# Optimization experiments

Measured on AMD Instinct MI355X. Metric: run time of the kernel, lower is better.

Reference implementation:

```python
import jax, jax.numpy as jnp
import numpy as np

B, S, D, HID, H, VOCAB, DFF = 4, 2048, 512, 512, 8, 32000, 2048
DK = HID // H   # per-head Q/K dim
DV = D // H     # per-head V dim


def sinusoidal_pe(L, d):
    pos = jnp.arange(L, dtype=jnp.float32)[:, None]
    i = jnp.arange(d, dtype=jnp.float32)[None, :]
    ang = pos / jnp.power(jnp.float32(10000.0), i / d)
    return jnp.where(jnp.arange(d)[None, :] % 2 == 0, jnp.sin(ang), jnp.cos(ang))  # [L, d]


def layer_norm(x, gamma, beta, eps=1e-5):
    mu = jnp.mean(x, axis=-1, keepdims=True)
    var = jnp.mean((x - mu) ** 2, axis=-1, keepdims=True)
    return (x - mu) * jax.lax.rsqrt(var + eps) * gamma + beta


def setup_inputs() -> dict:
    key = jax.random.key(0)
    ks = jax.random.split(key, 24)
    n = lambda k, shape, fan: jax.random.normal(k, shape, dtype=jnp.float32) / np.sqrt(fan)
    inp = {
        'x': jax.random.randint(ks[0], (B, S), 0, VOCAB),
        'emb': n(ks[1], (VOCAB, D), D),
        'WfQ': n(ks[2], (D, HID), D), 'bfQ': jnp.zeros((HID,), jnp.float32),
        'WfK': n(ks[3], (D, HID), D), 'bfK': jnp.zeros((HID,), jnp.float32),
        'WfV': n(ks[4], (D, D), D),   'bfV': jnp.zeros((D,), jnp.float32),
        'WQ': n(ks[5], (H, HID, DK), HID), 'bQ': jnp.zeros((H, DK), jnp.float32),
        'WK': n(ks[6], (H, HID, DK), HID), 'bK': jnp.zeros((H, DK), jnp.float32),
        'WV': n(ks[7], (H, D, DV), D),     'bV': jnp.zeros((H, DV), jnp.float32),
        'Wo': n(ks[8], (D, D), D),   'bo': jnp.zeros((D,), jnp.float32),
        'W1': n(ks[9], (D, DFF), D), 'b1': jnp.zeros((DFF,), jnp.float32),
        'W2': n(ks[10], (DFF, D), DFF), 'b2': jnp.zeros((D,), jnp.float32),
        'gamma': jnp.ones((D,), jnp.float32), 'beta': jnp.zeros((D,), jnp.float32),
    }
    return inp


def reference(x, emb, WfQ, bfQ, WfK, bfK, WfV, bfV, WQ, bQ, WK, bK, WV, bV,
              Wo, bo, W1, b1, W2, b2, gamma, beta):
    z = emb[x] + sinusoidal_pe(x.shape[1], D)[None]            # [B,S,D]
    Q = z @ WfQ + bfQ                                           # [B,S,HID]
    K = z @ WfK + bfK
    V = z @ WfV + bfV                                           # [B,S,D]
    # per-head projections (batched equivalent of the per-head Linear loop)
    Qh = jnp.einsum('bsd,hdk->bhsk', Q, WQ) + bQ[None, :, None, :]  # [B,H,S,DK]
    Kh = jnp.einsum('bsd,hdk->bhsk', K, WK) + bK[None, :, None, :]
    Vh = jnp.einsum('bsd,hdv->bhsv', V, WV) + bV[None, :, None, :]  # [B,H,S,DV]
    scores = jnp.einsum('bhqk,bhsk->bhqs', Qh, Kh) / np.sqrt(DK)    # [B,H,S,S]
    attn = jax.nn.softmax(scores, axis=-1)
    heads = jnp.einsum('bhqs,bhsv->bhqv', attn, Vh)                 # [B,H,S,DV]
    concat = heads.transpose(0, 2, 1, 3).reshape(x.shape[0], x.shape[1], D)
    attn_out = concat @ Wo + bo
    a = layer_norm(attn_out + z, gamma, beta)
    ffn = jax.nn.relu(a @ W1 + b1) @ W2 + b2
    out = layer_norm(ffn + a, gamma, beta)   # same (shared) LayerNorm params, as in source
    return jax.nn.relu(out)
```

## Files before the change

kernel.cpp:

```cpp
#include <hip/hip_runtime.h>
#include <math.h>

typedef __bf16 bf16;
typedef __bf16 bf16x8 __attribute__((ext_vector_type(8)));
typedef __bf16 bf16x4 __attribute__((ext_vector_type(4)));
typedef _Float16 f16;
typedef _Float16 f16x8 __attribute__((ext_vector_type(8)));
typedef _Float16 f16x4 __attribute__((ext_vector_type(4)));
typedef _Float16 f16x2 __attribute__((ext_vector_type(2)));
typedef __fp16 h16x2 __attribute__((ext_vector_type(2)));
typedef float f32x4 __attribute__((ext_vector_type(4)));
typedef unsigned int u32;

#define S_LEN 2048
#define QSCALE 0.18033688011112042f
#define FIXEDMAX 8.0f

__device__ __forceinline__ void gload_lds16(const void* g, void* l) {
  __builtin_amdgcn_global_load_lds((const __attribute__((address_space(1))) u32*)g,
                                   (__attribute__((address_space(3))) u32*)l, 16, 0, 0);
}

__global__ __launch_bounds__(256) void embed_pe(const int* __restrict__ x,
    const float* __restrict__ emb, float* __restrict__ zf, bf16* __restrict__ zb)
{
  const int row = blockIdx.x;
  const int s = row & (S_LEN - 1);
  const int tok = x[row];
  const float* e = emb + (size_t)tok * 512;
  float* zr = zf + (size_t)row * 512;
  bf16* zbr = zb + (size_t)row * 512;
  for (int i = threadIdx.x; i < 512; i += 256) {
    float invf = __expf((float)i * (-9.210340371976184f / 512.0f));
    float ang = (float)s * invf;
    float pe = (i & 1) ? __cosf(ang) : __sinf(ang);
    float v = e[i] + pe;
    zr[i] = v;
    zbr[i] = (bf16)v;
  }
}

__global__ __launch_bounds__(256) void conv_all(
    const float* __restrict__ WfQ, const float* __restrict__ WfK, const float* __restrict__ WfV,
    const float* __restrict__ WQ, const float* __restrict__ WK, const float* __restrict__ WV,
    const float* __restrict__ Wo, const float* __restrict__ W1, const float* __restrict__ W2,
    bf16* __restrict__ wfqp, bf16* __restrict__ wfkp, bf16* __restrict__ wfvp,
    bf16* __restrict__ wqt, bf16* __restrict__ wkt, bf16* __restrict__ wvt,
    bf16* __restrict__ wot, bf16* __restrict__ w1t, bf16* __restrict__ w2t)
{
  int gid = blockIdx.x * 256 + threadIdx.x;
  int y = blockIdx.y;
  if (y < 3) {
    if (gid >= 262144) return;
    const float* in = y == 0 ? WfQ : (y == 1 ? WfK : WfV);
    bf16* out = y == 0 ? wfqp : (y == 1 ? wfkp : wfvp);
    out[gid] = (bf16)in[gid];
  } else if (y < 6) {
    if (gid >= 262144) return;
    const float* in = y == 3 ? WQ : (y == 4 ? WK : WV);
    bf16* out = y == 3 ? wqt : (y == 4 ? wkt : wvt);
    float scale = y == 3 ? QSCALE : 1.0f;
    int r = gid & 511, t = gid >> 9, c = t & 63, h = t >> 6;
    out[gid] = (bf16)(in[((size_t)(h * 512 + r)) * 64 + c] * scale);
  } else if (y == 6) {
    if (gid >= 262144) return;
    int r = gid & 511, c = gid >> 9;
    wot[gid] = (bf16)Wo[r * 512 + c];
  } else if (y == 7) {
    int r = gid & 511, c = gid >> 9;
    w1t[gid] = (bf16)W1[r * 2048 + c];
  } else {
    int r = gid & 2047, c = gid >> 11;
    w2t[gid] = (bf16)W2[r * 512 + c];
  }
}

__global__ __launch_bounds__(256) void bias_comb(
    const float* __restrict__ bfQ, const float* __restrict__ bfK, const float* __restrict__ bfV,
    const float* __restrict__ WQ, const float* __restrict__ WK, const float* __restrict__ WV,
    const float* __restrict__ bQ, const float* __restrict__ bK, const float* __restrict__ bV,
    float* __restrict__ bc)
{
  int n = blockIdx.x * 4 + (threadIdx.x >> 6);
  int lane = threadIdx.x & 63;
  int z = n >> 9, hk = n & 511, h = hk >> 6, k = hk & 63;
  const float* bf = z == 0 ? bfQ : (z == 1 ? bfK : bfV);
  const float* W  = z == 0 ? WQ  : (z == 1 ? WK  : WV);
  const float* bH = z == 0 ? bQ  : (z == 1 ? bK  : bV);
  float s = 0.f;
  for (int e = lane; e < 512; e += 64)
    s += bf[e] * W[((size_t)h * 512 + e) * 64 + k];
  #pragma unroll
  for (int m = 1; m < 64; m <<= 1) s += __shfl_xor(s, m, 64);
  if (lane == 0) {
    float v = s + bH[h * 64 + k];
    if (z == 0) v *= QSCALE;
    bc[n] = v;
  }
}

__global__ __launch_bounds__(256) void gemm_comb(
    const bf16* __restrict__ wqt, const bf16* __restrict__ wkt, const bf16* __restrict__ wvt,
    const bf16* __restrict__ wfqp, const bf16* __restrict__ wfkp, const bf16* __restrict__ wfvp,
    bf16* __restrict__ wc)
{
  __shared__ bf16 As[128 * 32];
  __shared__ bf16 Bs[64 * 32];
  const int z = blockIdx.z;
  const bf16* A  = z == 0 ? wqt : (z == 1 ? wkt : wvt);
  const bf16* Bt = z == 0 ? wfqp : (z == 1 ? wfkp : wfvp);
  bf16* outb = wc + (size_t)z * 262144;
  const int tid = threadIdx.x;
  const int wave = tid >> 6, lane = tid & 63, quad = lane >> 4, l16 = lane & 15;
  const int row0 = blockIdx.x * 128, col0 = blockIdx.y * 64;
  const int wm = wave >> 1, wn = wave & 1;
  f32x4 acc[4][2] = {};

  for (int kk = 0; kk < 512; kk += 32) {
    __syncthreads();
    #pragma unroll
    for (int r = 0; r < 2; r++) {
      int c = r * 256 + tid;
      gload_lds16(A + (size_t)(row0 + (c >> 2)) * 512 + kk + (c & 3) * 8, As + c * 8);
    }
    gload_lds16(Bt + (size_t)(col0 + (tid >> 2)) * 512 + kk + (tid & 3) * 8, Bs + tid * 8);
    __syncthreads();
    bf16x8 af[4], bfr[2];
    #pragma unroll
    for (int i = 0; i < 4; i++)
      af[i] = *(const bf16x8*)(As + (wm * 64 + i * 16 + l16) * 32 + quad * 8);
    #pragma unroll
    for (int i = 0; i < 2; i++)
      bfr[i] = *(const bf16x8*)(Bs + (wn * 32 + i * 16 + l16) * 32 + quad * 8);
    #pragma unroll
    for (int mt = 0; mt < 4; mt++)
      #pragma unroll
      for (int nt = 0; nt < 2; nt++)
        acc[mt][nt] = __builtin_amdgcn_mfma_f32_16x16x32_bf16(af[mt], bfr[nt], acc[mt][nt], 0, 0, 0);
  }
  #pragma unroll
  for (int nt = 0; nt < 2; nt++) {
    int col = col0 + wn * 32 + nt * 16 + l16;
    #pragma unroll
    for (int mt = 0; mt < 4; mt++) {
      int rowb = row0 + wm * 64 + mt * 16 + quad * 4;
      #pragma unroll
      for (int i = 0; i < 4; i++)
        outb[(size_t)(rowb + i) * 512 + col] = (bf16)acc[mt][nt][i];
    }
  }
}

__global__ __launch_bounds__(256) void gemm_bt(
    const bf16* __restrict__ A, const bf16* __restrict__ Bt,
    const float* __restrict__ bias, bf16* __restrict__ outb,
    int M, int N, int K, int relu)
{
  __shared__ bf16 As[128 * 32];
  __shared__ bf16 Bs[128 * 32];
  const int tid = threadIdx.x;
  const int wave = tid >> 6, lane = tid & 63, quad = lane >> 4, l16 = lane & 15;
  const int row0 = blockIdx.x * 128, col0 = blockIdx.y * 128;
  const int wm = wave >> 1, wn = wave & 1;
  f32x4 acc[4][4] = {};

  for (int kk = 0; kk < K; kk += 32) {
    __syncthreads();
    #pragma unroll
    for (int r = 0; r < 2; r++) {
      int c = r * 256 + tid;
      gload_lds16(A + (size_t)(row0 + (c >> 2)) * K + kk + (c & 3) * 8, As + c * 8);
    }
    #pragma unroll
    for (int r = 0; r < 2; r++) {
      int c = r * 256 + tid;
      gload_lds16(Bt + (size_t)(col0 + (c >> 2)) * K + kk + (c & 3) * 8, Bs + c * 8);
    }
    __syncthreads();
    bf16x8 af[4], bfr[4];
    #pragma unroll
    for (int i = 0; i < 4; i++)
      af[i] = *(const bf16x8*)(As + (wm * 64 + i * 16 + l16) * 32 + quad * 8);
    #pragma unroll
    for (int i = 0; i < 4; i++)
      bfr[i] = *(const bf16x8*)(Bs + (wn * 64 + i * 16 + l16) * 32 + quad * 8);
    #pragma unroll
    for (int mt = 0; mt < 4; mt++)
      #pragma unroll
      for (int nt = 0; nt < 4; nt++)
        acc[mt][nt] = __builtin_amdgcn_mfma_f32_16x16x32_bf16(af[mt], bfr[nt], acc[mt][nt], 0, 0, 0);
  }

  #pragma unroll
  for (int nt = 0; nt < 4; nt++) {
    int col = col0 + wn * 64 + nt * 16 + l16;
    float bv = bias[col];
    #pragma unroll
    for (int mt = 0; mt < 4; mt++) {
      int rowb = row0 + wm * 64 + mt * 16 + quad * 4;
      #pragma unroll
      for (int i = 0; i < 4; i++) {
        float v = acc[mt][nt][i] + bv;
        if (relu) v = fmaxf(v, 0.f);
        outb[(size_t)(rowb + i) * N + col] = (bf16)v;
      }
    }
  }
}

__global__ __launch_bounds__(256) void gemm_qkv(
    const bf16* __restrict__ A, const bf16* __restrict__ Bt,
    const float* __restrict__ bias, f16* __restrict__ qk, f16* __restrict__ Vt)
{
  __shared__ bf16 As[128 * 32];
  __shared__ bf16 Bs[128 * 32];
  const int tid = threadIdx.x;
  const int wave = tid >> 6, lane = tid & 63, quad = lane >> 4, l16 = lane & 15;
  const int row0 = blockIdx.x * 128, col0 = blockIdx.y * 128;
  const int wm = wave >> 1, wn = wave & 1;
  f32x4 acc[4][4] = {};

  for (int kk = 0; kk < 512; kk += 32) {
    __syncthreads();
    #pragma unroll
    for (int r = 0; r < 2; r++) {
      int c = r * 256 + tid;
      gload_lds16(A + (size_t)(row0 + (c >> 2)) * 512 + kk + (c & 3) * 8, As + c * 8);
    }
    #pragma unroll
    for (int r = 0; r < 2; r++) {
      int c = r * 256 + tid;
      gload_lds16(Bt + (size_t)(col0 + (c >> 2)) * 512 + kk + (c & 3) * 8, Bs + c * 8);
    }
    __syncthreads();
    bf16x8 af[4], bfr[4];
    #pragma unroll
    for (int i = 0; i < 4; i++)
      af[i] = *(const bf16x8*)(As + (wm * 64 + i * 16 + l16) * 32 + quad * 8);
    #pragma unroll
    for (int i = 0; i < 4; i++)
      bfr[i] = *(const bf16x8*)(Bs + (wn * 64 + i * 16 + l16) * 32 + quad * 8);
    #pragma unroll
    for (int mt = 0; mt < 4; mt++)
      #pragma unroll
      for (int nt = 0; nt < 4; nt++)
        acc[mt][nt] = __builtin_amdgcn_mfma_f32_16x16x32_bf16(af[mt], bfr[nt], acc[mt][nt], 0, 0, 0);
  }

  #pragma unroll
  for (int nt = 0; nt < 4; nt++) {
    int col = col0 + wn * 64 + nt * 16 + l16;
    float bv = bias[col];
    if (col < 1024) {
      #pragma unroll
      for (int mt = 0; mt < 4; mt++) {
        int rowb = row0 + wm * 64 + mt * 16 + quad * 4;
        #pragma unroll
        for (int i = 0; i < 4; i++)
          qk[(size_t)(rowb + i) * 1024 + col] = (f16)(acc[mt][nt][i] + bv);
      }
    } else {
      int h = (col - 1024) >> 6, dv = col & 63;
      #pragma unroll
      for (int mt = 0; mt < 4; mt++) {
        int rowb = row0 + wm * 64 + mt * 16 + quad * 4;
        int b = rowb >> 11, s = rowb & 2047;
        f16x4 vv;
        #pragma unroll
        for (int i = 0; i < 4; i++) vv[i] = (f16)(acc[mt][nt][i] + bv);
        *(f16x4*)(Vt + ((size_t)((b * 8 + h) * 64 + dv)) * 2048 + s) = vv;
      }
    }
  }
}

__global__ __launch_bounds__(256) void gemm_part(
    const bf16* __restrict__ A, const bf16* __restrict__ Bt,
    float* __restrict__ Pa, float* __restrict__ Pb, int N, int K, int Kh)
{
  __shared__ bf16 As[128 * 32];
  __shared__ bf16 Bs[128 * 32];
  const int tid = threadIdx.x;
  const int wave = tid >> 6, lane = tid & 63, quad = lane >> 4, l16 = lane & 15;
  const int row0 = blockIdx.x * 128, col0 = blockIdx.y * 128;
  const int wm = wave >> 1, wn = wave & 1;
  const int kk0 = blockIdx.z * Kh;
  float* P = blockIdx.z ? Pb : Pa;
  f32x4 acc[4][4] = {};

  for (int kk = kk0; kk < kk0 + Kh; kk += 32) {
    __syncthreads();
    #pragma unroll
    for (int r = 0; r < 2; r++) {
      int c = r * 256 + tid;
      gload_lds16(A + (size_t)(row0 + (c >> 2)) * K + kk + (c & 3) * 8, As + c * 8);
    }
    #pragma unroll
    for (int r = 0; r < 2; r++) {
      int c = r * 256 + tid;
      gload_lds16(Bt + (size_t)(col0 + (c >> 2)) * K + kk + (c & 3) * 8, Bs + c * 8);
    }
    __syncthreads();
    bf16x8 af[4], bfr[4];
    #pragma unroll
    for (int i = 0; i < 4; i++)
      af[i] = *(const bf16x8*)(As + (wm * 64 + i * 16 + l16) * 32 + quad * 8);
    #pragma unroll
    for (int i = 0; i < 4; i++)
      bfr[i] = *(const bf16x8*)(Bs + (wn * 64 + i * 16 + l16) * 32 + quad * 8);
    #pragma unroll
    for (int mt = 0; mt < 4; mt++)
      #pragma unroll
      for (int nt = 0; nt < 4; nt++)
        acc[mt][nt] = __builtin_amdgcn_mfma_f32_16x16x32_bf16(af[mt], bfr[nt], acc[mt][nt], 0, 0, 0);
  }

  #pragma unroll
  for (int nt = 0; nt < 4; nt++) {
    int col = col0 + wn * 64 + nt * 16 + l16;
    #pragma unroll
    for (int mt = 0; mt < 4; mt++) {
      int rowb = row0 + wm * 64 + mt * 16 + quad * 4;
      #pragma unroll
      for (int i = 0; i < 4; i++)
        P[(size_t)(rowb + i) * N + col] = acc[mt][nt][i];
    }
  }
}

__global__ __launch_bounds__(256) void flash_attn(
    const f16* __restrict__ qk, const f16* __restrict__ Vt,
    bf16* __restrict__ Op, float* __restrict__ Rp)
{
  __shared__ f16 Ks[2][4096];
  __shared__ f16 Vs[2][4096];
  const int bh = blockIdx.y, b = bh >> 3, h = bh & 7;
  const int q0 = blockIdx.x * 128;
  const int half = blockIdx.z;
  const int tid = threadIdx.x;
  const int wave = tid >> 6, lane = tid & 63, quad = lane >> 4, l16 = lane & 15;

  const f16* Qb = qk + ((size_t)b * S_LEN) * 1024 + h * 64;
  const f16* Kb = Qb + 512;
  const f16* Vtb = Vt + ((size_t)bh * 64) * 2048;
  const int key0 = half * 1024;

  f16x8 qf[2][2];
  #pragma unroll
  for (int f = 0; f < 2; f++) {
    int qrow = q0 + wave * 32 + f * 16 + l16;
    #pragma unroll
    for (int kh = 0; kh < 2; kh++)
      qf[f][kh] = *(const f16x8*)(Qb + (size_t)qrow * 1024 + kh * 32 + quad * 8);
  }

  f32x4 O[2][4] = {};
  f32x4 Osum[2] = {};
  const f16x4 onesA = {(f16)1.f, (f16)1.f, (f16)1.f, (f16)1.f};
  const int swz = l16 & 7;

  f16x8 kreg[2], vreg[2];
  const int srow = tid >> 3, soff = tid & 7;
  const int srow1 = srow + 32;

  {
    int kb = key0;
    kreg[0] = *(const f16x8*)(Kb + (size_t)(kb + srow) * 1024 + soff * 8);
    vreg[0] = *(const f16x8*)(Vtb + (size_t)srow * 2048 + kb + soff * 8);
    kreg[1] = *(const f16x8*)(Kb + (size_t)(kb + srow1) * 1024 + soff * 8);
    vreg[1] = *(const f16x8*)(Vtb + (size_t)srow1 * 2048 + kb + soff * 8);
  }

  for (int c = 0; c < 16; c++) {
    f16* KsB = Ks[c & 1];
    f16* VsB = Vs[c & 1];
    *(f16x8*)(KsB + srow * 64 + ((soff ^ (srow & 7)) * 8)) = kreg[0];
    *(f16x8*)(VsB + srow * 64 + ((soff ^ (srow & 7)) * 8)) = vreg[0];
    *(f16x8*)(KsB + srow1 * 64 + ((soff ^ (srow1 & 7)) * 8)) = kreg[1];
    *(f16x8*)(VsB + srow1 * 64 + ((soff ^ (srow1 & 7)) * 8)) = vreg[1];
    __syncthreads();
    if (c < 15) {
      int kb = key0 + (c + 1) * 64;
      kreg[0] = *(const f16x8*)(Kb + (size_t)(kb + srow) * 1024 + soff * 8);
      vreg[0] = *(const f16x8*)(Vtb + (size_t)srow * 2048 + kb + soff * 8);
      kreg[1] = *(const f16x8*)(Kb + (size_t)(kb + srow1) * 1024 + soff * 8);
      vreg[1] = *(const f16x8*)(Vtb + (size_t)srow1 * 2048 + kb + soff * 8);
    }

    #pragma unroll
    for (int nt = 0; nt < 4; nt++) {
      const f16* kp = KsB + (nt * 16 + l16) * 64;
      f16x8 kf0 = *(const f16x8*)(kp + ((quad ^ swz) * 8));
      f16x8 kf1 = *(const f16x8*)(kp + (((4 + quad) ^ swz) * 8));
      f16x4 pf[2];
      #pragma unroll
      for (int f = 0; f < 2; f++) {
        f32x4 a = {};
        a = __builtin_amdgcn_mfma_f32_16x16x32_f16(kf0, qf[f][0], a, 0, 0, 0);
        a = __builtin_amdgcn_mfma_f32_16x16x32_f16(kf1, qf[f][1], a, 0, 0, 0);
        float e0 = exp2f(a[0] - FIXEDMAX);
        float e1 = exp2f(a[1] - FIXEDMAX);
        float e2 = exp2f(a[2] - FIXEDMAX);
        float e3 = exp2f(a[3] - FIXEDMAX);
        h16x2 lo = __builtin_amdgcn_cvt_pkrtz(e0, e1);
        h16x2 hi = __builtin_amdgcn_cvt_pkrtz(e2, e3);
        f16x2 lo2 = __builtin_bit_cast(f16x2, lo);
        f16x2 hi2 = __builtin_bit_cast(f16x2, hi);
        pf[f] = __builtin_shufflevector(lo2, hi2, 0, 1, 2, 3);
        Osum[f] = __builtin_amdgcn_mfma_f32_16x16x16f16(onesA, pf[f], Osum[f], 0, 0, 0);
      }
      int vchunk = nt * 2 + (quad >> 1);
      #pragma unroll
      for (int mt = 0; mt < 4; mt++) {
        const f16* vp = VsB + (mt * 16 + l16) * 64 + ((vchunk ^ swz) * 8) + (quad & 1) * 4;
        f16x4 vf = *(const f16x4*)vp;
        #pragma unroll
        for (int f = 0; f < 2; f++)
          O[f][mt] = __builtin_amdgcn_mfma_f32_16x16x16f16(vf, pf[f], O[f][mt], 0, 0, 0);
      }
    }
    __syncthreads();
  }

  #pragma unroll
  for (int f = 0; f < 2; f++) {
    bf16* ob = (f == 0 ? (bf16*)&Ks[0][0] : (bf16*)&Vs[0][0]) + wave * 1152;
    #pragma unroll
    for (int mt = 0; mt < 4; mt++)
      #pragma unroll
      for (int i = 0; i < 4; i++)
        ob[l16 * 72 + mt * 16 + quad * 4 + i] = (bf16)O[f][mt][i];
  }
  asm volatile("s_waitcnt lgkmcnt(0)" ::: "memory");
  const size_t obase = (size_t)(half * 32 + bh) * 2048;
  #pragma unroll
  for (int f = 0; f < 2; f++) {
    bf16* ob = (f == 0 ? (bf16*)&Ks[0][0] : (bf16*)&Vs[0][0]) + wave * 1152;
    int row = lane >> 2, dvb = (lane & 3) * 16;
    bf16x8 o0 = *(const bf16x8*)(ob + row * 72 + dvb);
    bf16x8 o1 = *(const bf16x8*)(ob + row * 72 + dvb + 8);
    size_t g = (obase + q0 + wave * 32 + f * 16 + row) * 64 + dvb;
    *(bf16x8*)(Op + g) = o0;
    *(bf16x8*)(Op + g + 8) = o1;
    if (quad == f)
      Rp[obase + q0 + wave * 32 + f * 16 + l16] = Osum[f][0];
  }
}

__global__ __launch_bounds__(256) void attn_merge(const bf16* __restrict__ Op,
    const float* __restrict__ Rp, bf16* __restrict__ concat)
{
  int t = blockIdx.x * 256 + threadIdx.x;
  int dv4 = t & 15, s = (t >> 4) & 2047, bh = t >> 15;
  int rb = bh * 2048 + s;
  float r = Rp[rb] + Rp[65536 + rb];
  float inv = 1.f / r;
  size_t ia = ((size_t)bh * 2048 + s) * 64 + dv4 * 4;
  bf16x4 a = *(const bf16x4*)(Op + ia);
  bf16x4 c = *(const bf16x4*)(Op + 4194304ull + ia);
  bf16x4 o;
  #pragma unroll
  for (int i = 0; i < 4; i++) o[i] = (bf16)(((float)a[i] + (float)c[i]) * inv);
  int b = bh >> 3, h = bh & 7;
  *(bf16x4*)(concat + ((size_t)(b * 2048 + s)) * 512 + h * 64 + dv4 * 4) = o;
}

__global__ __launch_bounds__(256) void ln_merge(const float* __restrict__ Pa,
    const float* __restrict__ Pb, const float* __restrict__ badd,
    const float* __restrict__ resid, const float* __restrict__ gamma,
    const float* __restrict__ beta, float* __restrict__ outf,
    bf16* __restrict__ outb, int relu)
{
  const int row = blockIdx.x * 4 + (threadIdx.x >> 6);
  const int lane = threadIdx.x & 63;
  const size_t base = (size_t)row * 512;
  const float4* pa = (const float4*)(Pa + base);
  const float4* pb = (const float4*)(Pb + base);
  const float4* rr = (const float4*)(resid + base);
  const float4* bb = (const float4*)badd;
  float4 A0 = pa[lane], A1 = pa[lane + 64];
  float4 B0 = pb[lane], B1 = pb[lane + 64];
  float4 R0 = rr[lane], R1 = rr[lane + 64];
  float4 C0 = bb[lane], C1 = bb[lane + 64];
  float4 v0 = {A0.x+B0.x+R0.x+C0.x, A0.y+B0.y+R0.y+C0.y, A0.z+B0.z+R0.z+C0.z, A0.w+B0.w+R0.w+C0.w};
  float4 v1 = {A1.x+B1.x+R1.x+C1.x, A1.y+B1.y+R1.y+C1.y, A1.z+B1.z+R1.z+C1.z, A1.w+B1.w+R1.w+C1.w};
  float s = v0.x + v0.y + v0.z + v0.w + v1.x + v1.y + v1.z + v1.w;
  #pragma unroll
  for (int m = 1; m < 64; m <<= 1) s += __shfl_xor(s, m, 64);
  float mu = s * (1.f / 512.f);
  float d0 = v0.x - mu, d1 = v0.y - mu, d2 = v0.z - mu, d3 = v0.w - mu;
  float d4 = v1.x - mu, d5 = v1.y - mu, d6 = v1.z - mu, d7 = v1.w - mu;
  float q = d0*d0 + d1*d1 + d2*d2 + d3*d3 + d4*d4 + d5*d5 + d6*d6 + d7*d7;
  #pragma unroll
  for (int m = 1; m < 64; m <<= 1) q += __shfl_xor(q, m, 64);
  float rs = rsqrtf(q * (1.f / 512.f) + 1e-5f);
  const float4* gp = (const float4*)gamma;
  const float4* bp = (const float4*)beta;
  float4 g0 = gp[lane], g1 = gp[lane + 64];
  float4 b0 = bp[lane], b1 = bp[lane + 64];
  float y0 = d0 * rs * g0.x + b0.x, y1 = d1 * rs * g0.y + b0.y;
  float y2 = d2 * rs * g0.z + b0.z, y3 = d3 * rs * g0.w + b0.w;
  float y4 = d4 * rs * g1.x + b1.x, y5 = d5 * rs * g1.y + b1.y;
  float y6 = d6 * rs * g1.z + b1.z, y7 = d7 * rs * g1.w + b1.w;
  if (relu) {
    y0 = fmaxf(y0, 0.f); y1 = fmaxf(y1, 0.f); y2 = fmaxf(y2, 0.f); y3 = fmaxf(y3, 0.f);
    y4 = fmaxf(y4, 0.f); y5 = fmaxf(y5, 0.f); y6 = fmaxf(y6, 0.f); y7 = fmaxf(y7, 0.f);
  }
  float4* op = (float4*)(outf + base);
  float4 o0 = {y0, y1, y2, y3}, o1 = {y4, y5, y6, y7};
  op[lane] = o0;
  op[lane + 64] = o1;
  if (outb) {
    bf16x4 c0 = {(bf16)y0, (bf16)y1, (bf16)y2, (bf16)y3};
    bf16x4 c1 = {(bf16)y4, (bf16)y5, (bf16)y6, (bf16)y7};
    *(bf16x4*)(outb + base + lane * 4) = c0;
    *(bf16x4*)(outb + base + 256 + lane * 4) = c1;
  }
}

extern "C" void kernel_launch(void* const* d_in, const int* in_sizes, int n_in,
                              void* d_out, int out_size, void* d_ws, size_t ws_size,
                              hipStream_t stream)
{
  const int*   x    = (const int*)  d_in[0];
  const float* emb  = (const float*)d_in[1];
  const float* WfQ  = (const float*)d_in[2];
  const float* bfQv = (const float*)d_in[3];
  const float* WfK  = (const float*)d_in[4];
  const float* bfKv = (const float*)d_in[5];
  const float* WfV  = (const float*)d_in[6];
  const float* bfVv = (const float*)d_in[7];
  const float* WQ   = (const float*)d_in[8];
  const float* bQ   = (const float*)d_in[9];
  const float* WK   = (const float*)d_in[10];
  const float* bK   = (const float*)d_in[11];
  const float* WV   = (const float*)d_in[12];
  const float* bV   = (const float*)d_in[13];
  const float* Wo   = (const float*)d_in[14];
  const float* bo   = (const float*)d_in[15];
  const float* W1   = (const float*)d_in[16];
  const float* b1   = (const float*)d_in[17];
  const float* W2   = (const float*)d_in[18];
  const float* b2   = (const float*)d_in[19];
  const float* gamma= (const float*)d_in[20];
  const float* beta = (const float*)d_in[21];
  float* out = (float*)d_out;

  char* ws = (char*)d_ws;
  const size_t MB = 1024ull * 1024;
  float* zf   = (float*)(ws);
  bf16*  bz   = (bf16*) (ws + 16 * MB);
  f16*   qkh  = (f16*)  (ws + 24 * MB);
  f16*   Vt   = (f16*)  (ws + 40 * MB);
  bf16*  Op   = (bf16*) (ws + 48 * MB);
  float* Rp   = (float*)(ws + 80 * MB);
  bf16*  concat = (bf16*)(ws + 82 * MB);
  float* PaW  = (float*)(ws + 48 * MB);
  float* PbW  = (float*)(ws + 64 * MB);
  bf16*  ffn1 = (bf16*) (ws + 24 * MB);
  float* Pa2  = (float*)(ws + 56 * MB);
  float* Pb2  = (float*)(ws + 72 * MB);
  char* wp = ws + 90 * MB;
  bf16* wfqp = (bf16*)(wp);
  bf16* wfkp = (bf16*)(wp + 512 * 1024);
  bf16* wfvp = (bf16*)(wp + 1024 * 1024);
  bf16* wqt  = (bf16*)(wp + 1536 * 1024);
  bf16* wkt  = (bf16*)(wp + 2048 * 1024);
  bf16* wvt  = (bf16*)(wp + 2560 * 1024);
  bf16* wc   = (bf16*)(wp + 3072 * 1024);
  bf16* wot  = (bf16*)(wp + 4608 * 1024);
  bf16* w1t  = (bf16*)(wp + 5120 * 1024);
  bf16* w2t  = (bf16*)(wp + 7168 * 1024);
  float* bc  = (float*)(wp + 9216 * 1024);

  conv_all<<<dim3(4096, 9), 256, 0, stream>>>(WfQ, WfK, WfV, WQ, WK, WV, Wo, W1, W2,
                                              wfqp, wfkp, wfvp, wqt, wkt, wvt, wot, w1t, w2t);
  bias_comb<<<384, 256, 0, stream>>>(bfQv, bfKv, bfVv, WQ, WK, WV, bQ, bK, bV, bc);
  gemm_comb<<<dim3(4, 8, 3), 256, 0, stream>>>(wqt, wkt, wvt, wfqp, wfkp, wfvp, wc);

  embed_pe<<<8192, 256, 0, stream>>>(x, emb, zf, bz);

  gemm_qkv<<<dim3(64, 12), 256, 0, stream>>>(bz, wc, bc, qkh, Vt);
  flash_attn<<<dim3(16, 32, 2), 256, 0, stream>>>(qkh, Vt, Op, Rp);
  attn_merge<<<4096, 256, 0, stream>>>(Op, Rp, concat);

  gemm_part<<<dim3(64, 4, 2), 256, 0, stream>>>(concat, wot, PaW, PbW, 512, 512, 256);
  ln_merge<<<2048, 256, 0, stream>>>(PaW, PbW, bo, zf, gamma, beta, zf, bz, 0);
  gemm_bt<<<dim3(64, 16), 256, 0, stream>>>(bz, w1t, b1, ffn1, 8192, 2048, 512, 1);
  gemm_part<<<dim3(64, 4, 2), 256, 0, stream>>>(ffn1, w2t, Pa2, Pb2, 512, 2048, 1024);
  ln_merge<<<2048, 256, 0, stream>>>(Pa2, Pb2, b2, zf, gamma, beta, out, nullptr, 1);
}
```

Before: 376.2 us.

## Double-buffer GEMM tiles via register prefetch and store split-K partials in bf16

Replaces the direct global-to-LDS loads in all three GEMM kernels with a shared macro. It prefetches the next K-slice into registers while the current slice is consumed from a double-buffered LDS tile, which removes one barrier per iteration and hides load latency. Split-K partials are now written and read as bf16 instead of fp32, halving partial-sum traffic into the LayerNorm merge, which is rewritten to read 8 contiguous elements per lane. The fixed max offset in the attention exp2 is also dropped. That raises the risk of fp16 overflow in the probabilities and loses precision in the partial sums.

```diff
diff --git a/kernel.cpp b/kernel.cpp
--- a/kernel.cpp
+++ b/kernel.cpp
@@ -14,7 +14,6 @@
 
 #define S_LEN 2048
 #define QSCALE 0.18033688011112042f
-#define FIXEDMAX 8.0f
 
 __device__ __forceinline__ void gload_lds16(const void* g, void* l) {
   __builtin_amdgcn_global_load_lds((const __attribute__((address_space(1))) u32*)g,
@@ -151,45 +150,59 @@
   }
 }
 
+#define GEMM_CORE(A_, Bt_, K_, KK0_, ITERS_)                                            \
+  bf16x8 ar0, ar1, br0, br1;                                                            \
+  const int c0 = tid, c1 = 256 + tid;                                                   \
+  const size_t aoff0 = (size_t)(row0 + (c0 >> 2)) * (K_) + (c0 & 3) * 8;                \
+  const size_t aoff1 = (size_t)(row0 + (c1 >> 2)) * (K_) + (c1 & 3) * 8;                \
+  const size_t boff0 = (size_t)(col0 + (c0 >> 2)) * (K_) + (c0 & 3) * 8;                \
+  const size_t boff1 = (size_t)(col0 + (c1 >> 2)) * (K_) + (c1 & 3) * 8;                \
+  ar0 = *(const bf16x8*)((A_) + aoff0 + (KK0_));                                        \
+  ar1 = *(const bf16x8*)((A_) + aoff1 + (KK0_));                                        \
+  br0 = *(const bf16x8*)((Bt_) + boff0 + (KK0_));                                       \
+  br1 = *(const bf16x8*)((Bt_) + boff1 + (KK0_));                                       \
+  for (int it = 0; it < (ITERS_); it++) {                                               \
+    bf16* AsB = As[it & 1];                                                             \
+    bf16* BsB = Bs[it & 1];                                                             \
+    *(bf16x8*)(AsB + c0 * 8) = ar0;                                                     \
+    *(bf16x8*)(AsB + c1 * 8) = ar1;                                                     \
+    *(bf16x8*)(BsB + c0 * 8) = br0;                                                     \
+    *(bf16x8*)(BsB + c1 * 8) = br1;                                                     \
+    __syncthreads();                                                                    \
+    if (it + 1 < (ITERS_)) {                                                            \
+      int kk = (KK0_) + (it + 1) * 32;                                                  \
+      ar0 = *(const bf16x8*)((A_) + aoff0 + kk);                                        \
+      ar1 = *(const bf16x8*)((A_) + aoff1 + kk);                                        \
+      br0 = *(const bf16x8*)((Bt_) + boff0 + kk);                                       \
+      br1 = *(const bf16x8*)((Bt_) + boff1 + kk);                                       \
+    }                                                                                   \
+    bf16x8 af[4], bfr[4];                                                               \
+    _Pragma("unroll")                                                                   \
+    for (int i = 0; i < 4; i++)                                                         \
+      af[i] = *(const bf16x8*)(AsB + (wm * 64 + i * 16 + l16) * 32 + quad * 8);         \
+    _Pragma("unroll")                                                                   \
+    for (int i = 0; i < 4; i++)                                                         \
+      bfr[i] = *(const bf16x8*)(BsB + (wn * 64 + i * 16 + l16) * 32 + quad * 8);        \
+    _Pragma("unroll")                                                                   \
+    for (int mt = 0; mt < 4; mt++)                                                      \
+      _Pragma("unroll")                                                                 \
+      for (int nt = 0; nt < 4; nt++)                                                    \
+        acc[mt][nt] = __builtin_amdgcn_mfma_f32_16x16x32_bf16(af[mt], bfr[nt], acc[mt][nt], 0, 0, 0); \
+  }
+
 __global__ __launch_bounds__(256) void gemm_bt(
     const bf16* __restrict__ A, const bf16* __restrict__ Bt,
     const float* __restrict__ bias, bf16* __restrict__ outb,
     int M, int N, int K, int relu)
 {
-  __shared__ bf16 As[128 * 32];
-  __shared__ bf16 Bs[128 * 32];
+  __shared__ bf16 As[2][4096];
+  __shared__ bf16 Bs[2][4096];
   const int tid = threadIdx.x;
   const int wave = tid >> 6, lane = tid & 63, quad = lane >> 4, l16 = lane & 15;
   const int row0 = blockIdx.x * 128, col0 = blockIdx.y * 128;
   const int wm = wave >> 1, wn = wave & 1;
   f32x4 acc[4][4] = {};
-
-  for (int kk = 0; kk < K; kk += 32) {
-    __syncthreads();
-    #pragma unroll
-    for (int r = 0; r < 2; r++) {
-      int c = r * 256 + tid;
-      gload_lds16(A + (size_t)(row0 + (c >> 2)) * K + kk + (c & 3) * 8, As + c * 8);
-    }
-    #pragma unroll
-    for (int r = 0; r < 2; r++) {
-      int c = r * 256 + tid;
-      gload_lds16(Bt + (size_t)(col0 + (c >> 2)) * K + kk + (c & 3) * 8, Bs + c * 8);
-    }
-    __syncthreads();
-    bf16x8 af[4], bfr[4];
-    #pragma unroll
-    for (int i = 0; i < 4; i++)
-      af[i] = *(const bf16x8*)(As + (wm * 64 + i * 16 + l16) * 32 + quad * 8);
-    #pragma unroll
-    for (int i = 0; i < 4; i++)
-      bfr[i] = *(const bf16x8*)(Bs + (wn * 64 + i * 16 + l16) * 32 + quad * 8);
-    #pragma unroll
-    for (int mt = 0; mt < 4; mt++)
-      #pragma unroll
-      for (int nt = 0; nt < 4; nt++)
-        acc[mt][nt] = __builtin_amdgcn_mfma_f32_16x16x32_bf16(af[mt], bfr[nt], acc[mt][nt], 0, 0, 0);
-  }
+  GEMM_CORE(A, Bt, K, 0, K / 32)
 
   #pragma unroll
   for (int nt = 0; nt < 4; nt++) {
@@ -212,40 +225,14 @@
     const bf16* __restrict__ A, const bf16* __restrict__ Bt,
     const float* __restrict__ bias, f16* __restrict__ qk, f16* __restrict__ Vt)
 {
-  __shared__ bf16 As[128 * 32];
-  __shared__ bf16 Bs[128 * 32];
+  __shared__ bf16 As[2][4096];
+  __shared__ bf16 Bs[2][4096];
   const int tid = threadIdx.x;
   const int wave = tid >> 6, lane = tid & 63, quad = lane >> 4, l16 = lane & 15;
   const int row0 = blockIdx.x * 128, col0 = blockIdx.y * 128;
   const int wm = wave >> 1, wn = wave & 1;
   f32x4 acc[4][4] = {};
-
-  for (int kk = 0; kk < 512; kk += 32) {
-    __syncthreads();
-    #pragma unroll
-    for (int r = 0; r < 2; r++) {
-      int c = r * 256 + tid;
-      gload_lds16(A + (size_t)(row0 + (c >> 2)) * 512 + kk + (c & 3) * 8, As + c * 8);
-    }
-    #pragma unroll
-    for (int r = 0; r < 2; r++) {
-      int c = r * 256 + tid;
-      gload_lds16(Bt + (size_t)(col0 + (c >> 2)) * 512 + kk + (c & 3) * 8, Bs + c * 8);
-    }
-    __syncthreads();
-    bf16x8 af[4], bfr[4];
-    #pragma unroll
-    for (int i = 0; i < 4; i++)
-      af[i] = *(const bf16x8*)(As + (wm * 64 + i * 16 + l16) * 32 + quad * 8);
-    #pragma unroll
-    for (int i = 0; i < 4; i++)
-      bfr[i] = *(const bf16x8*)(Bs + (wn * 64 + i * 16 + l16) * 32 + quad * 8);
-    #pragma unroll
-    for (int mt = 0; mt < 4; mt++)
-      #pragma unroll
-      for (int nt = 0; nt < 4; nt++)
-        acc[mt][nt] = __builtin_amdgcn_mfma_f32_16x16x32_bf16(af[mt], bfr[nt], acc[mt][nt], 0, 0, 0);
-  }
+  GEMM_CORE(A, Bt, 512, 0, 16)
 
   #pragma unroll
   for (int nt = 0; nt < 4; nt++) {
@@ -276,44 +263,18 @@
 
 __global__ __launch_bounds__(256) void gemm_part(
     const bf16* __restrict__ A, const bf16* __restrict__ Bt,
-    float* __restrict__ Pa, float* __restrict__ Pb, int N, int K, int Kh)
-{
-  __shared__ bf16 As[128 * 32];
-  __shared__ bf16 Bs[128 * 32];
+    bf16* __restrict__ Pa, bf16* __restrict__ Pb, int N, int K, int Kh)
+{
+  __shared__ bf16 As[2][4096];
+  __shared__ bf16 Bs[2][4096];
   const int tid = threadIdx.x;
   const int wave = tid >> 6, lane = tid & 63, quad = lane >> 4, l16 = lane & 15;
   const int row0 = blockIdx.x * 128, col0 = blockIdx.y * 128;
   const int wm = wave >> 1, wn = wave & 1;
   const int kk0 = blockIdx.z * Kh;
-  float* P = blockIdx.z ? Pb : Pa;
+  bf16* P = blockIdx.z ? Pb : Pa;
   f32x4 acc[4][4] = {};
-
-  for (int kk = kk0; kk < kk0 + Kh; kk += 32) {
-    __syncthreads();
-    #pragma unroll
-    for (int r = 0; r < 2; r++) {
-      int c = r * 256 + tid;
-      gload_lds16(A + (size_t)(row0 + (c >> 2)) * K + kk + (c & 3) * 8, As + c * 8);
-    }
-    #pragma unroll
-    for (int r = 0; r < 2; r++) {
-      int c = r * 256 + tid;
-      gload_lds16(Bt + (size_t)(col0 + (c >> 2)) * K + kk + (c & 3) * 8, Bs + c * 8);
-    }
-    __syncthreads();
-    bf16x8 af[4], bfr[4];
-    #pragma unroll
-    for (int i = 0; i < 4; i++)
-      af[i] = *(const bf16x8*)(As + (wm * 64 + i * 16 + l16) * 32 + quad * 8);
-    #pragma unroll
-    for (int i = 0; i < 4; i++)
-      bfr[i] = *(const bf16x8*)(Bs + (wn * 64 + i * 16 + l16) * 32 + quad * 8);
-    #pragma unroll
-    for (int mt = 0; mt < 4; mt++)
-      #pragma unroll
-      for (int nt = 0; nt < 4; nt++)
-        acc[mt][nt] = __builtin_amdgcn_mfma_f32_16x16x32_bf16(af[mt], bfr[nt], acc[mt][nt], 0, 0, 0);
-  }
+  GEMM_CORE(A, Bt, K, kk0, Kh / 32)
 
   #pragma unroll
   for (int nt = 0; nt < 4; nt++) {
@@ -323,7 +284,7 @@
       int rowb = row0 + wm * 64 + mt * 16 + quad * 4;
       #pragma unroll
       for (int i = 0; i < 4; i++)
-        P[(size_t)(rowb + i) * N + col] = acc[mt][nt][i];
+        P[(size_t)(rowb + i) * N + col] = (bf16)acc[mt][nt][i];
     }
   }
 }
@@ -398,10 +359,10 @@
         f32x4 a = {};
         a = __builtin_amdgcn_mfma_f32_16x16x32_f16(kf0, qf[f][0], a, 0, 0, 0);
         a = __builtin_amdgcn_mfma_f32_16x16x32_f16(kf1, qf[f][1], a, 0, 0, 0);
-        float e0 = exp2f(a[0] - FIXEDMAX);
-        float e1 = exp2f(a[1] - FIXEDMAX);
-        float e2 = exp2f(a[2] - FIXEDMAX);
-        float e3 = exp2f(a[3] - FIXEDMAX);
+        float e0 = exp2f(a[0]);
+        float e1 = exp2f(a[1]);
+        float e2 = exp2f(a[2]);
+        float e3 = exp2f(a[3]);
         h16x2 lo = __builtin_amdgcn_cvt_pkrtz(e0, e1);
         h16x2 hi = __builtin_amdgcn_cvt_pkrtz(e2, e3);
         f16x2 lo2 = __builtin_bit_cast(f16x2, lo);
@@ -465,8 +426,8 @@
   *(bf16x4*)(concat + ((size_t)(b * 2048 + s)) * 512 + h * 64 + dv4 * 4) = o;
 }
 
-__global__ __launch_bounds__(256) void ln_merge(const float* __restrict__ Pa,
-    const float* __restrict__ Pb, const float* __restrict__ badd,
+__global__ __launch_bounds__(256) void ln_merge(const bf16* __restrict__ Pa,
+    const bf16* __restrict__ Pb, const float* __restrict__ badd,
     const float* __restrict__ resid, const float* __restrict__ gamma,
     const float* __restrict__ beta, float* __restrict__ outf,
     bf16* __restrict__ outb, int relu)
@@ -474,47 +435,55 @@
   const int row = blockIdx.x * 4 + (threadIdx.x >> 6);
   const int lane = threadIdx.x & 63;
   const size_t base = (size_t)row * 512;
-  const float4* pa = (const float4*)(Pa + base);
-  const float4* pb = (const float4*)(Pb + base);
-  const float4* rr = (const float4*)(resid + base);
-  const float4* bb = (const float4*)badd;
-  float4 A0 = pa[lane], A1 = pa[lane + 64];
-  float4 B0 = pb[lane], B1 = pb[lane + 64];
-  float4 R0 = rr[lane], R1 = rr[lane + 64];
-  float4 C0 = bb[lane], C1 = bb[lane + 64];
-  float4 v0 = {A0.x+B0.x+R0.x+C0.x, A0.y+B0.y+R0.y+C0.y, A0.z+B0.z+R0.z+C0.z, A0.w+B0.w+R0.w+C0.w};
-  float4 v1 = {A1.x+B1.x+R1.x+C1.x, A1.y+B1.y+R1.y+C1.y, A1.z+B1.z+R1.z+C1.z, A1.w+B1.w+R1.w+C1.w};
-  float s = v0.x + v0.y + v0.z + v0.w + v1.x + v1.y + v1.z + v1.w;
+  const int e0 = lane * 8;
+  bf16x8 pa = *(const bf16x8*)(Pa + base + e0);
+  bf16x8 pb = *(const bf16x8*)(Pb + base + e0);
+  float4 R0 = *(const float4*)(resid + base + e0);
+  float4 R1 = *(const float4*)(resid + base + e0 + 4);
+  float4 C0 = *(const float4*)(badd + e0);
+  float4 C1 = *(const float4*)(badd + e0 + 4);
+  float v[8];
+  v[0] = (float)pa[0] + (float)pb[0] + R0.x + C0.x;
+  v[1] = (float)pa[1] + (float)pb[1] + R0.y + C0.y;
+  v[2] = (float)pa[2] + (float)pb[2] + R0.z + C0.z;
+  v[3] = (float)pa[3] + (float)pb[3] + R0.w + C0.w;
+  v[4] = (float)pa[4] + (float)pb[4] + R1.x + C1.x;
+  v[5] = (float)pa[5] + (float)pb[5] + R1.y + C1.y;
+  v[6] = (float)pa[6] + (float)pb[6] + R1.z + C1.z;
+  v[7] = (float)pa[7] + (float)pb[7] + R1.w + C1.w;
+  float s = 0.f;
+  #pragma unroll
+  for (int i = 0; i < 8; i++) s += v[i];
   #pragma unroll
   for (int m = 1; m < 64; m <<= 1) s += __shfl_xor(s, m, 64);
   float mu = s * (1.f / 512.f);
-  float d0 = v0.x - mu, d1 = v0.y - mu, d2 = v0.z - mu, d3 = v0.w - mu;
-  float d4 = v1.x - mu, d5 = v1.y - mu, d6 = v1.z - mu, d7 = v1.w - mu;
-  float q = d0*d0 + d1*d1 + d2*d2 + d3*d3 + d4*d4 + d5*d5 + d6*d6 + d7*d7;
+  float d[8], q = 0.f;
+  #pragma unroll
+  for (int i = 0; i < 8; i++) { d[i] = v[i] - mu; q += d[i] * d[i]; }
   #pragma unroll
   for (int m = 1; m < 64; m <<= 1) q += __shfl_xor(q, m, 64);
   float rs = rsqrtf(q * (1.f / 512.f) + 1e-5f);
-  const float4* gp = (const float4*)gamma;
-  const float4* bp = (const float4*)beta;
-  float4 g0 = gp[lane], g1 = gp[lane + 64];
-  float4 b0 = bp[lane], b1 = bp[lane + 64];
-  float y0 = d0 * rs * g0.x + b0.x, y1 = d1 * rs * g0.y + b0.y;
-  float y2 = d2 * rs * g0.z + b0.z, y3 = d3 * rs * g0.w + b0.w;
-  float y4 = d4 * rs * g1.x + b1.x, y5 = d5 * rs * g1.y + b1.y;
-  float y6 = d6 * rs * g1.z + b1.z, y7 = d7 * rs * g1.w + b1.w;
+  float4 g0 = *(const float4*)(gamma + e0);
+  float4 g1 = *(const float4*)(gamma + e0 + 4);
+  float4 b0 = *(const float4*)(beta + e0);
+  float4 b1 = *(const float4*)(beta + e0 + 4);
+  float y[8];
+  y[0] = d[0] * rs * g0.x + b0.x; y[1] = d[1] * rs * g0.y + b0.y;
+  y[2] = d[2] * rs * g0.z + b0.z; y[3] = d[3] * rs * g0.w + b0.w;
+  y[4] = d[4] * rs * g1.x + b1.x; y[5] = d[5] * rs * g1.y + b1.y;
+  y[6] = d[6] * rs * g1.z + b1.z; y[7] = d[7] * rs * g1.w + b1.w;
   if (relu) {
-    y0 = fmaxf(y0, 0.f); y1 = fmaxf(y1, 0.f); y2 = fmaxf(y2, 0.f); y3 = fmaxf(y3, 0.f);
-    y4 = fmaxf(y4, 0.f); y5 = fmaxf(y5, 0.f); y6 = fmaxf(y6, 0.f); y7 = fmaxf(y7, 0.f);
-  }
-  float4* op = (float4*)(outf + base);
-  float4 o0 = {y0, y1, y2, y3}, o1 = {y4, y5, y6, y7};
-  op[lane] = o0;
-  op[lane + 64] = o1;
+    #pragma unroll
+    for (int i = 0; i < 8; i++) y[i] = fmaxf(y[i], 0.f);
+  }
+  float4 o0 = {y[0], y[1], y[2], y[3]}, o1 = {y[4], y[5], y[6], y[7]};
+  *(float4*)(outf + base + e0) = o0;
+  *(float4*)(outf + base + e0 + 4) = o1;
   if (outb) {
-    bf16x4 c0 = {(bf16)y0, (bf16)y1, (bf16)y2, (bf16)y3};
-    bf16x4 c1 = {(bf16)y4, (bf16)y5, (bf16)y6, (bf16)y7};
-    *(bf16x4*)(outb + base + lane * 4) = c0;
-    *(bf16x4*)(outb + base + 256 + lane * 4) = c1;
+    bf16x8 ob;
+    #pragma unroll
+    for (int i = 0; i < 8; i++) ob[i] = (bf16)y[i];
+    *(bf16x8*)(outb + base + e0) = ob;
   }
 }
 
@@ -555,11 +524,11 @@
   bf16*  Op   = (bf16*) (ws + 48 * MB);
   float* Rp   = (float*)(ws + 80 * MB);
   bf16*  concat = (bf16*)(ws + 82 * MB);
-  float* PaW  = (float*)(ws + 48 * MB);
-  float* PbW  = (float*)(ws + 64 * MB);
+  bf16*  PaW  = (bf16*) (ws + 48 * MB);
+  bf16*  PbW  = (bf16*) (ws + 56 * MB);
   bf16*  ffn1 = (bf16*) (ws + 24 * MB);
-  float* Pa2  = (float*)(ws + 56 * MB);
-  float* Pb2  = (float*)(ws + 72 * MB);
+  bf16*  Pa2  = (bf16*) (ws + 56 * MB);
+  bf16*  Pb2  = (bf16*) (ws + 64 * MB);
   char* wp = ws + 90 * MB;
   bf16* wfqp = (bf16*)(wp);
   bf16* wfkp = (bf16*)(wp + 512 * 1024);
```

After: 358.5 us. 4.7% less time.
